# Optimization experiments

Hardware: AMD Instinct MI355X
Metric: run time of the kernel (lower is better)

The kernel has to match this reference:

```python
import jax, jax.numpy as jnp
import numpy as np

B, I, J, P, D = 64, 512, 512, 32, 8
EPS = 1e-5


def _std(t):
    # standardize over last two dims; torch.std uses ddof=1 (unbiased)
    m = t.mean(axis=(-1, -2), keepdims=True)
    s = t.std(axis=(-1, -2), keepdims=True, ddof=1)
    return (t - m) / (s + EPS)


def _flat_softmax(t):
    # softmax over the flattened trailing two dims (torch: flatten(1).softmax(1))
    sh = t.shape
    return jax.nn.softmax(t.reshape(sh[0], sh[1], -1), axis=-1).reshape(sh)


def setup_inputs() -> dict:
    key = jax.random.key(0)
    ks = jax.random.split(key, 10)

    def xav(k, shape):
        # xavier_uniform with relu gain, fan over last two dims
        fan_in, fan_out = shape[-2], shape[-1]
        lim = float(np.sqrt(2.0) * np.sqrt(6.0 / (fan_in + fan_out)))
        return jax.random.uniform(k, shape, jnp.float32, -lim, lim)

    return {
        "x": jax.random.normal(ks[0], (B, I, J), jnp.float32),
        "o_xj": xav(ks[1], (D, J, P)),
        "o_xi": xav(ks[2], (D, I, P)),
        "p_xj": xav(ks[3], (D, I, P)),
        "p_xi": xav(ks[4], (D, J, P)),
        "rel_o_xj": xav(ks[5], (D, J, P)),
        "rel_o_xi": xav(ks[6], (D, I, P)),
        "rel_p_xj": xav(ks[7], (D, P, P)),
        "rel_p_xi": xav(ks[8], (D, P, P)),
        "gamma": jnp.ones((D, 1), jnp.float32),
        "beta": jnp.zeros((D, 1), jnp.float32),
    }


def reference(x, o_xj, o_xi, p_xj, p_xi, rel_o_xj, rel_o_xi, rel_p_xj, rel_p_xi, gamma, beta):
    # Eval-mode reference: dropout is identity. Depth loop vectorized via a leading d axis.
    scale = (I / P) * (J / P)
    x_mean = x.mean(axis=(-1, -2), keepdims=True)[:, None] * scale  # [B,1,1,1]
    x_std = x.std(axis=(-1, -2), keepdims=True, ddof=1)[:, None] * scale

    # relative-mass terms on the original input
    o_rel_xj_sum = _flat_softmax(jnp.einsum('bij,djp->bdip', x, rel_o_xj)).sum(-2)  # [B,D,P]
    o_rel_xi_sum = _flat_softmax(jnp.einsum('bij,dip->bdjp', x, rel_o_xi)).sum(-2)  # [B,D,P]

    # original transforms
    o_t_xj = _std(jnp.tanh(jnp.einsum('bij,djp->bdip', x, o_xj)))   # [B,D,I,P]
    o_t_xi = _std(jnp.tanh(jnp.einsum('bij,dip->bdjp', x, o_xi)))   # [B,D,J,P]

    # permuted transforms -> [B,D,P,P]
    p_t_xj = _std(jnp.tanh(jnp.einsum('bdip,diq->bdpq', o_t_xj, p_xj)))
    p_t_xi = _std(jnp.tanh(jnp.einsum('bdjp,djq->bdqp', o_t_xi, p_xi)))

    # relative-mass terms on the projected tensors
    p_rel_xj_sum = _flat_softmax(jnp.einsum('bdpq,dqr->bdpr', p_t_xj, rel_p_xj)).sum(-2)
    p_rel_xi_sum = _flat_softmax(jnp.einsum('bdpq,dqr->bdpr', p_t_xi, rel_p_xi)).sum(-2)

    fj = jnp.sqrt(o_rel_xj_sum / p_rel_xj_sum)[..., None]  # [B,D,P,1]
    fi = jnp.sqrt(o_rel_xi_sum / p_rel_xi_sum)[..., None]

    xb = jnp.tanh((p_t_xj * fj) * jnp.swapaxes(p_t_xi * fi, -1, -2))
    xb = _std(xb) * x_std + x_mean
    xb = xb * gamma[None, :, :, None] + beta[None, :, :, None]
    return xb.sum(axis=1) / D  # [B,P,P]
```

## Files before the change

kernel.cpp:

```cpp
#include <hip/hip_runtime.h>
#include <math.h>

static constexpr float EPSF = 1e-5f;

typedef short bf16x8 __attribute__((ext_vector_type(8)));
typedef float f32x4 __attribute__((ext_vector_type(4)));
typedef ushort u16x8 __attribute__((ext_vector_type(8)));

__device__ inline ushort bf16rn(float f) {
  unsigned u = __float_as_uint(f);
  unsigned r = (u + 0x7FFFu + ((u >> 16) & 1u)) >> 16;
  return (ushort)r;
}
__device__ inline float bf2f(ushort u) { return __uint_as_float(((unsigned)u) << 16); }
__device__ inline void split2(float f, ushort& hi, ushort& lo) {
  ushort h = bf16rn(f);
  float hf = bf2f(h);
  hi = h;
  lo = bf16rn(f - hf);
}
__device__ inline float fast_tanh(float x) {
  float e = __expf(2.f * x);
  return 1.f - 2.f * __builtin_amdgcn_rcpf(e + 1.f);
}

__device__ inline void gload16(const ushort* g, ushort* l) {
  __builtin_amdgcn_global_load_lds((const __attribute__((address_space(1))) void*)g,
                                   (__attribute__((address_space(3))) void*)l, 16, 0, 0);
}

__device__ inline size_t tiled_addr(int row, int k) {
  return (size_t)(row >> 7) * 65536 + (size_t)(k >> 5) * 4096 +
         (size_t)((k >> 3) & 3) * 1024 + (size_t)(row & 127) * 8 + (k & 7);
}

__global__ __launch_bounds__(256) void conv_pack(
    const float* __restrict__ x,
    const float* __restrict__ o_xj, const float* __restrict__ o_xi,
    const float* __restrict__ rel_o_xj, const float* __restrict__ rel_o_xi,
    const float* __restrict__ p_xj, const float* __restrict__ p_xi,
    ushort* __restrict__ xhi, ushort* __restrict__ xthi,
    ushort* __restrict__ wjhi, ushort* __restrict__ wjlo,
    ushort* __restrict__ wihi, ushort* __restrict__ wilo,
    ushort* __restrict__ Wthi, ushort* __restrict__ Wtlo,
    float* __restrict__ colWs,
    float* __restrict__ bpart) {
  const int bx = blockIdx.x;
  const int tid = threadIdx.x;
  if (bx >= 4352) {
    const int pd = bx - 4352;
    const int path = pd >> 3, d = pd & 7;
    const float* src = (path ? p_xi : p_xj) + (size_t)d * 16384;
    ushort* whi = Wthi + (size_t)pd * 16384;
    ushort* wlo = Wtlo + (size_t)pd * 16384;
    __shared__ float buf[64][33];
    float cw = 0.f;
    const int q = tid >> 3, je8 = (tid & 7) * 8;
    for (int j0 = 0; j0 < 512; j0 += 64) {
      for (int l = tid; l < 2048; l += 256) buf[l >> 5][l & 31] = src[(size_t)j0 * 32 + l];
      __syncthreads();
      u16x8 h8, l8;
      #pragma unroll
      for (int e = 0; e < 8; ++e) {
        float fv = buf[je8 + e][q];
        cw += fv;
        ushort h, l; split2(fv, h, l);
        h8[e] = h; l8[e] = l;
      }
      *reinterpret_cast<u16x8*>(&whi[(size_t)q * 512 + j0 + je8]) = h8;
      *reinterpret_cast<u16x8*>(&wlo[(size_t)q * 512 + j0 + je8]) = l8;
      __syncthreads();
    }
    cw += __shfl_xor(cw, 1); cw += __shfl_xor(cw, 2); cw += __shfl_xor(cw, 4);
    if ((tid & 7) == 0) colWs[(size_t)pd * 32 + q] = cw;
    return;
  }
  if (bx >= 4096) {
    int u = (bx - 4096) * 256 + tid;
    int path = u >> 15;
    int v = u & 32767;
    int c = v >> 6;
    int k0 = (v & 63) * 8;
    int d = c >> 6, s = (c >> 5) & 1, p = c & 31;
    const float* src = path ? (s ? rel_o_xi : o_xi) : (s ? rel_o_xj : o_xj);
    u16x8 h8, l8;
    #pragma unroll
    for (int e = 0; e < 8; ++e) {
      ushort h, l;
      split2(src[((size_t)d * 512 + k0 + e) * 32 + p], h, l);
      h8[e] = h; l8[e] = l;
    }
    size_t a = tiled_addr(c, k0);
    ushort* whi = path ? wihi : wjhi;
    ushort* wlo = path ? wilo : wjlo;
    *reinterpret_cast<u16x8*>(&whi[a]) = h8;
    *reinterpret_cast<u16x8*>(&wlo[a]) = l8;
    return;
  }
  __shared__ float tile[64][65];
  __shared__ float rs[256], rs2[256];
  const int ti = bx & 7, tj = (bx >> 3) & 7, b = bx >> 6;
  const int i0 = ti * 64, j0 = tj * 64;
  const float* xb = x + (size_t)b * 262144;
  const size_t obase = (size_t)b * 262144;
  const int tr = tid >> 4;
  const int tc = (tid & 15) * 4;
  float s = 0.f, s2 = 0.f;
  #pragma unroll
  for (int r = 0; r < 4; ++r) {
    const int row = r * 16 + tr;
    float4 v = *reinterpret_cast<const float4*>(&xb[(size_t)(i0 + row) * 512 + j0 + tc]);
    tile[row][tc + 0] = v.x; tile[row][tc + 1] = v.y;
    tile[row][tc + 2] = v.z; tile[row][tc + 3] = v.w;
    s += v.x + v.y + v.z + v.w;
    s2 += v.x * v.x + v.y * v.y + v.z * v.z + v.w * v.w;
  }
  __syncthreads();
  const int kg = tid >> 5;
  const int rp = tid & 31;
  #pragma unroll
  for (int rr = 0; rr < 2; ++rr) {
    const int li = rp + rr * 32;
    u16x8 h8;
    #pragma unroll
    for (int e = 0; e < 8; ++e) h8[e] = bf16rn(tile[li][kg * 8 + e]);
    *reinterpret_cast<u16x8*>(&xhi[obase + tiled_addr(i0 + li, j0 + kg * 8)]) = h8;
  }
  #pragma unroll
  for (int rr = 0; rr < 2; ++rr) {
    const int lj = rp + rr * 32;
    u16x8 h8;
    #pragma unroll
    for (int e = 0; e < 8; ++e) h8[e] = bf16rn(tile[kg * 8 + e][lj]);
    *reinterpret_cast<u16x8*>(&xthi[obase + tiled_addr(j0 + lj, i0 + kg * 8)]) = h8;
  }
  rs[tid] = s; rs2[tid] = s2;
  __syncthreads();
  for (int off = 128; off > 0; off >>= 1) {
    if (tid < off) { rs[tid] += rs[tid + off]; rs2[tid] += rs2[tid + off]; }
    __syncthreads();
  }
  if (tid == 0) {
    float* pb = bpart + ((size_t)b * 64 + tj * 8 + ti) * 2;
    pb[0] = rs[0]; pb[1] = rs2[0];
  }
}

__global__ __launch_bounds__(256) void mfma_gemm(
    const ushort* __restrict__ xhi, const ushort* __restrict__ xthi,
    const ushort* __restrict__ wjhi, const ushort* __restrict__ wjlo,
    const ushort* __restrict__ wihi, const ushort* __restrict__ wilo,
    ushort* __restrict__ Ttj, ushort* __restrict__ Tti,
    float* __restrict__ pJ, float* __restrict__ pI) {
  const int id = blockIdx.x;
  const int wid = (id & 7) * 256 + (id >> 3);
  const int ct = wid & 3, tm = (wid >> 2) & 3, bz = wid >> 4;
  const int b = bz >> 1, path = bz & 1;
  const ushort* Ahi = (path ? xthi : xhi) + (size_t)b * 262144 + (size_t)tm * 65536;
  const ushort* Bhi = (path ? wihi : wjhi) + (size_t)ct * 65536;
  const ushort* Blo = (path ? wilo : wjlo) + (size_t)ct * 65536;
  ushort* Tb = (path ? Tti : Ttj) + (size_t)b * 131072;
  float* partial = path ? pI : pJ;

  __shared__ alignas(16) ushort As_hi[4096], Bs_hi[4096], Bs_lo[4096];
  __shared__ float rsum[4], rsq[4], rcol[4][32];

  const int tid = threadIdx.x;
  const int lane = tid & 63, w = tid >> 6;
  const int wr = w >> 1, wc = w & 1;
  const int m0 = tm * 128;

  const int L8 = (w * 64 + lane) * 8;
  const int ldsb0 = (w * 64) * 8;
  const int ldsb1 = 2048 + (w * 64) * 8;

  f32x4 acc[4][4] = {};
  const int fr = lane & 15;
  const int kc = lane >> 4;

  for (int ks = 0; ks < 16; ++ks) {
    const ushort* Ah = Ahi + ks * 4096;
    const ushort* Bh = Bhi + ks * 4096;
    const ushort* Bl = Blo + ks * 4096;
    gload16(Ah + L8,        &As_hi[ldsb0]);
    gload16(Ah + 2048 + L8, &As_hi[ldsb1]);
    gload16(Bh + L8,        &Bs_hi[ldsb0]);
    gload16(Bh + 2048 + L8, &Bs_hi[ldsb1]);
    gload16(Bl + L8,        &Bs_lo[ldsb0]);
    gload16(Bl + 2048 + L8, &Bs_lo[ldsb1]);
    __syncthreads();
    bf16x8 ah[4], bh[4], bl2[2];
    #pragma unroll
    for (int mi = 0; mi < 4; ++mi) {
      const int ra = (kc * 128 + wr * 64 + mi * 16 + fr) * 8;
      ah[mi] = *reinterpret_cast<const bf16x8*>(&As_hi[ra]);
    }
    #pragma unroll
    for (int ni = 0; ni < 4; ++ni) {
      const int rb = (kc * 128 + wc * 64 + ni * 16 + fr) * 8;
      bh[ni] = *reinterpret_cast<const bf16x8*>(&Bs_hi[rb]);
      if (ni < 2) bl2[ni] = *reinterpret_cast<const bf16x8*>(&Bs_lo[rb]);
    }
    #pragma unroll
    for (int mi = 0; mi < 4; ++mi) {
      #pragma unroll
      for (int ni = 0; ni < 4; ++ni)
        acc[mi][ni] = __builtin_amdgcn_mfma_f32_16x16x32_bf16(ah[mi], bh[ni], acc[mi][ni], 0, 0, 0);
      #pragma unroll
      for (int ni = 0; ni < 2; ++ni)
        acc[mi][ni] = __builtin_amdgcn_mfma_f32_16x16x32_bf16(ah[mi], bl2[ni], acc[mi][ni], 0, 0, 0);
    }
    __syncthreads();
  }

  float lsum = 0.f, lsq = 0.f, cs0 = 0.f, cs1 = 0.f;
  const int d = ct * 2 + wc;
  #pragma unroll
  for (int mi = 0; mi < 4; ++mi) {
    const int rbase = m0 + wr * 64 + mi * 16 + ((lane >> 4) << 2);
    #pragma unroll
    for (int ni = 0; ni < 4; ++ni) {
      if (ni < 2) {
        const int p = ni * 16 + fr;
        float t0 = fast_tanh(acc[mi][ni][0]);
        float t1 = fast_tanh(acc[mi][ni][1]);
        float t2 = fast_tanh(acc[mi][ni][2]);
        float t3 = fast_tanh(acc[mi][ni][3]);
        lsum += t0 + t1 + t2 + t3;
        lsq += t0 * t0 + t1 * t1 + t2 * t2 + t3 * t3;
        ushort4 pk;
        pk.x = bf16rn(t0); pk.y = bf16rn(t1); pk.z = bf16rn(t2); pk.w = bf16rn(t3);
        *reinterpret_cast<ushort4*>(&Tb[((size_t)d * 32 + p) * 512 + rbase]) = pk;
      } else {
        #pragma unroll
        for (int r = 0; r < 4; ++r) {
          float e = __expf(acc[mi][ni][r]);
          if (ni == 2) cs0 += e; else cs1 += e;
        }
      }
    }
  }
  #pragma unroll
  for (int m = 1; m < 64; m <<= 1) { lsum += __shfl_xor(lsum, m); lsq += __shfl_xor(lsq, m); }
  cs0 += __shfl_xor(cs0, 16); cs0 += __shfl_xor(cs0, 32);
  cs1 += __shfl_xor(cs1, 16); cs1 += __shfl_xor(cs1, 32);
  if (lane == 0) { rsum[w] = lsum; rsq[w] = lsq; }
  if (lane < 16) { rcol[w][lane] = cs0; rcol[w][16 + lane] = cs1; }
  __syncthreads();
  if (tid < 64) {
    const int wc2 = tid >> 5, p = tid & 31;
    float* pb = partial + (((size_t)b * 4 + tm) * 8 + ct * 2 + wc2) * 34;
    pb[2 + p] = rcol[wc2][p] + rcol[wc2 + 2][p];
    if (p == 0) {
      pb[0] = rsum[wc2] + rsum[wc2 + 2];
      pb[1] = rsq[wc2] + rsq[wc2 + 2];
    }
  }
}

__global__ void reduce_stats_kernel(const float* __restrict__ pJ, const float* __restrict__ pI,
                                    float* __restrict__ stats) {
  const int bd = blockIdx.x;
  const int b = bd >> 3, d = bd & 7;
  const int t = threadIdx.x;
  __shared__ float tmp[2][34];
  if (t < 34) {
    float v = 0.f;
    for (int tm = 0; tm < 4; ++tm) v += pJ[(((size_t)b * 4 + tm) * 8 + d) * 34 + t];
    tmp[0][t] = v;
  } else if (t >= 64 && t < 98) {
    const int u = t - 64;
    float v = 0.f;
    for (int tm = 0; tm < 4; ++tm) v += pI[(((size_t)b * 4 + tm) * 8 + d) * 34 + u];
    tmp[1][u] = v;
  }
  __syncthreads();
  if (t < 2) {
    const float* tp = tmp[t];
    float* st = stats + (size_t)bd * 68;
    const float N = 16384.f;
    float mean = tp[0] / N;
    float var = (tp[1] - tp[0] * tp[0] / N) / (N - 1.f);
    float rstd = 1.f / (sqrtf(fmaxf(var, 0.f)) + EPSF);
    st[t * 2 + 0] = mean;
    st[t * 2 + 1] = rstd;
    float tot = 0.f;
    for (int k = 0; k < 32; ++k) tot += tp[2 + k];
    float inv = 1.f / tot;
    for (int k = 0; k < 32; ++k) st[4 + t * 32 + k] = tp[2 + k] * inv;
  }
}

__global__ __launch_bounds__(256) void stage3_fused(
    const ushort* __restrict__ Ttj, const ushort* __restrict__ Tti,
    const ushort* __restrict__ Wthi, const ushort* __restrict__ Wtlo,
    const float* __restrict__ colWs,
    const float* __restrict__ rel_pj, const float* __restrict__ rel_pi,
    const float* __restrict__ stats, const float* __restrict__ bpart,
    const float* __restrict__ gamma_p, const float* __restrict__ beta_p,
    float* __restrict__ xball) {
  const int bd = blockIdx.x;
  const int b = bd >> 3, d = bd & 7;
  const int tid = threadIdx.x;
  const int lane = tid & 63, w = tid >> 6;
  const int path = w >> 1, mt = w & 1;
  const int fr = lane & 15, kg = lane >> 4;

  __shared__ float Vl[2][32][33];
  __shared__ float Rl[2][32][32];
  __shared__ float cred[2][32][33];
  __shared__ float colw_s[64];
  __shared__ float pred[4][2];
  __shared__ float csum[2][32];
  __shared__ float stot[2];
  __shared__ float fsc[2][32];
  __shared__ float red[256], red2[256];
  __shared__ float sred[2], sbst[2];

  for (int l = tid; l < 2048; l += 256) {
    const int pp = l >> 10, idx = l & 1023;
    const float* Rsrc = pp ? rel_pi : rel_pj;
    Rl[pp][idx >> 5][idx & 31] = Rsrc[(size_t)d * 1024 + idx];
  }
  if (tid < 64) colw_s[tid] = colWs[(((size_t)(tid >> 5) * 8 + d)) * 32 + (tid & 31)];
  if (tid >= 128 && tid < 192) {
    const int t = tid - 128;
    float s = bpart[(size_t)b * 128 + t * 2];
    float s2 = bpart[(size_t)b * 128 + t * 2 + 1];
    #pragma unroll
    for (int m = 1; m < 64; m <<= 1) { s += __shfl_xor(s, m); s2 += __shfl_xor(s2, m); }
    if (t == 0) {
      const float N = 262144.f;
      float mean = s / N;
      float var = (s2 - s * s / N) / (N - 1.f);
      sbst[0] = mean * 256.f;
      sbst[1] = sqrtf(fmaxf(var, 0.f)) * 256.f;
    }
  }
  __syncthreads();

  f32x4 acc0 = {}, acc1 = {};
  const ushort* Whi_p = Wthi + ((size_t)path * 8 + d) * 16384;
  const ushort* Wlo_p = Wtlo + ((size_t)path * 8 + d) * 16384;
  const ushort* Tp = (path ? Tti : Ttj) + ((size_t)b * 8 + d) * 16384;

  if (path == 0) {
    const ushort* Arow = Tp + (size_t)(mt * 16 + fr) * 512;
    const ushort* B0h = Whi_p + (size_t)fr * 512;
    const ushort* B0l = Wlo_p + (size_t)fr * 512;
    const ushort* B1h = Whi_p + (size_t)(16 + fr) * 512;
    const ushort* B1l = Wlo_p + (size_t)(16 + fr) * 512;
    for (int k0 = 0; k0 < 512; k0 += 32) {
      const int ko = k0 + kg * 8;
      bf16x8 a   = *reinterpret_cast<const bf16x8*>(Arow + ko);
      bf16x8 b0h = *reinterpret_cast<const bf16x8*>(B0h + ko);
      bf16x8 b0l = *reinterpret_cast<const bf16x8*>(B0l + ko);
      bf16x8 b1h = *reinterpret_cast<const bf16x8*>(B1h + ko);
      bf16x8 b1l = *reinterpret_cast<const bf16x8*>(B1l + ko);
      acc0 = __builtin_amdgcn_mfma_f32_16x16x32_bf16(a, b0h, acc0, 0, 0, 0);
      acc0 = __builtin_amdgcn_mfma_f32_16x16x32_bf16(a, b0l, acc0, 0, 0, 0);
      acc1 = __builtin_amdgcn_mfma_f32_16x16x32_bf16(a, b1h, acc1, 0, 0, 0);
      acc1 = __builtin_amdgcn_mfma_f32_16x16x32_bf16(a, b1l, acc1, 0, 0, 0);
    }
  } else {
    const ushort* Ahr = Whi_p + (size_t)(mt * 16 + fr) * 512;
    const ushort* Alr = Wlo_p + (size_t)(mt * 16 + fr) * 512;
    const ushort* B0 = Tp + (size_t)fr * 512;
    const ushort* B1 = Tp + (size_t)(16 + fr) * 512;
    for (int k0 = 0; k0 < 512; k0 += 32) {
      const int ko = k0 + kg * 8;
      bf16x8 ah = *reinterpret_cast<const bf16x8*>(Ahr + ko);
      bf16x8 al = *reinterpret_cast<const bf16x8*>(Alr + ko);
      bf16x8 b0 = *reinterpret_cast<const bf16x8*>(B0 + ko);
      bf16x8 b1 = *reinterpret_cast<const bf16x8*>(B1 + ko);
      acc0 = __builtin_amdgcn_mfma_f32_16x16x32_bf16(ah, b0, acc0, 0, 0, 0);
      acc0 = __builtin_amdgcn_mfma_f32_16x16x32_bf16(al, b0, acc0, 0, 0, 0);
      acc1 = __builtin_amdgcn_mfma_f32_16x16x32_bf16(ah, b1, acc1, 0, 0, 0);
      acc1 = __builtin_amdgcn_mfma_f32_16x16x32_bf16(al, b1, acc1, 0, 0, 0);
    }
  }

  const float* st = stats + (size_t)bd * 68;
  const float mean = st[path * 2], rstd = st[path * 2 + 1];
  float tv0[4], tv1[4];
  float ls = 0.f, lq = 0.f;
  #pragma unroll
  for (int r = 0; r < 4; ++r) {
    const int rowm = mt * 16 + kg * 4 + r;
    {
      const int col = fr;
      const float cw = (path == 0) ? colw_s[col] : colw_s[32 + rowm];
      float t = fast_tanh((acc0[r] - mean * cw) * rstd);
      tv0[r] = t; ls += t; lq += t * t;
    }
    {
      const int col = 16 + fr;
      const float cw = (path == 0) ? colw_s[col] : colw_s[32 + rowm];
      float t = fast_tanh((acc1[r] - mean * cw) * rstd);
      tv1[r] = t; ls += t; lq += t * t;
    }
  }
  #pragma unroll
  for (int m = 1; m < 64; m <<= 1) { ls += __shfl_xor(ls, m); lq += __shfl_xor(lq, m); }
  if (lane == 0) { pred[w][0] = ls; pred[w][1] = lq; }
  __syncthreads();
  {
    const float S = pred[path * 2][0] + pred[path * 2 + 1][0];
    const float SS = pred[path * 2][1] + pred[path * 2 + 1][1];
    const float m2 = S / 1024.f;
    const float var = (SS - S * S / 1024.f) / 1023.f;
    const float r2 = 1.f / (sqrtf(fmaxf(var, 0.f)) + EPSF);
    #pragma unroll
    for (int r = 0; r < 4; ++r) {
      const int rowm = mt * 16 + kg * 4 + r;
      Vl[path][rowm][fr] = (tv0[r] - m2) * r2;
      Vl[path][rowm][16 + fr] = (tv1[r] - m2) * r2;
    }
  }
  __syncthreads();

  {
    const int t2 = tid & 127;
    const int prow = t2 >> 2, c8 = (t2 & 3) * 8;
    float racc[8] = {};
    #pragma unroll
    for (int c = 0; c < 32; ++c) {
      const float v = Vl[path][prow][c];
      #pragma unroll
      for (int e = 0; e < 8; ++e) racc[e] = fmaf(v, Rl[path][c][c8 + e], racc[e]);
    }
    #pragma unroll
    for (int e = 0; e < 8; ++e) cred[path][prow][c8 + e] = __expf(racc[e]);
  }
  __syncthreads();
  if (tid < 64) {
    const int pp = tid >> 5, q = tid & 31;
    float s = 0.f;
    #pragma unroll 8
    for (int p = 0; p < 32; ++p) s += cred[pp][p][q];
    csum[pp][q] = s;
  }
  __syncthreads();
  if (tid < 2) {
    float tot = 0.f;
    for (int k = 0; k < 32; ++k) tot += csum[tid][k];
    stot[tid] = tot;
  }
  __syncthreads();
  if (tid < 64) {
    const int pp = tid >> 5, q = tid & 31;
    fsc[pp][q] = sqrtf(st[4 + pp * 32 + q] * stot[pp] / csum[pp][q]);
  }
  __syncthreads();

  const int row = tid >> 3, c4 = (tid & 7) * 4;
  float xv[4]; float ls2 = 0.f, lq2 = 0.f;
  #pragma unroll
  for (int e = 0; e < 4; ++e) {
    const int q = c4 + e;
    float v = fast_tanh(Vl[0][row][q] * fsc[0][row] * Vl[1][q][row] * fsc[1][q]);
    xv[e] = v; ls2 += v; lq2 += v * v;
  }
  red[tid] = ls2; red2[tid] = lq2;
  __syncthreads();
  for (int off = 128; off > 0; off >>= 1) {
    if (tid < off) { red[tid] += red[tid + off]; red2[tid] += red2[tid + off]; }
    __syncthreads();
  }
  if (tid == 0) {
    float s = red[0], ss = red2[0];
    float m = s / 1024.f;
    float var = (ss - s * s / 1024.f) / 1023.f;
    sred[0] = m; sred[1] = 1.f / (sqrtf(fmaxf(var, 0.f)) + EPSF);
  }
  __syncthreads();
  const float m3 = sred[0], r3 = sred[1];
  const float xm = sbst[0], xs = sbst[1];
  const float g = gamma_p[d], be = beta_p[d];
  #pragma unroll
  for (int e = 0; e < 4; ++e) {
    float v = (xv[e] - m3) * r3 * xs + xm;
    xball[(size_t)bd * 1024 + row * 32 + c4 + e] = v * g + be;
  }
}

__global__ void final_kernel(const float* __restrict__ xball, float* __restrict__ out) {
  const int b = blockIdx.x;
  for (int e = threadIdx.x; e < 1024; e += 256) {
    float s = 0.f;
    #pragma unroll
    for (int d = 0; d < 8; ++d) s += xball[((size_t)(b * 8 + d)) * 1024 + e];
    out[(size_t)b * 1024 + e] = s * 0.125f;
  }
}

extern "C" void kernel_launch(void* const* d_in, const int* in_sizes, int n_in,
                              void* d_out, int out_size, void* d_ws, size_t ws_size,
                              hipStream_t stream) {
  const float* x        = (const float*)d_in[0];
  const float* o_xj     = (const float*)d_in[1];
  const float* o_xi     = (const float*)d_in[2];
  const float* p_xj     = (const float*)d_in[3];
  const float* p_xi     = (const float*)d_in[4];
  const float* rel_o_xj = (const float*)d_in[5];
  const float* rel_o_xi = (const float*)d_in[6];
  const float* rel_p_xj = (const float*)d_in[7];
  const float* rel_p_xi = (const float*)d_in[8];
  const float* gamma_p  = (const float*)d_in[9];
  const float* beta_p   = (const float*)d_in[10];
  float* out = (float*)d_out;

  char* base = (char*)d_ws;
  ushort* xhi  = (ushort*)base; base += (size_t)33554432;
  ushort* xthi = (ushort*)base; base += (size_t)33554432;
  ushort* wjhi = (ushort*)base; base += 524288;
  ushort* wjlo = (ushort*)base; base += 524288;
  ushort* wihi = (ushort*)base; base += 524288;
  ushort* wilo = (ushort*)base; base += 524288;
  ushort* Ttj  = (ushort*)base; base += (size_t)16777216;
  ushort* Tti  = (ushort*)base; base += (size_t)16777216;
  ushort* Wthi = (ushort*)base; base += 524288;
  ushort* Wtlo = (ushort*)base; base += 524288;
  float* colWs = (float*)base;  base += 2048;
  float* pJ    = (float*)base;  base += 278528;
  float* pI    = (float*)base;  base += 278528;
  float* bpart = (float*)base;  base += 32768;
  float* stats = (float*)base;  base += 139264;
  float* xball = (float*)base;  base += 2097152;

  hipLaunchKernelGGL(conv_pack, dim3(4368), dim3(256), 0, stream,
                     x, o_xj, o_xi, rel_o_xj, rel_o_xi, p_xj, p_xi,
                     xhi, xthi, wjhi, wjlo, wihi, wilo, Wthi, Wtlo, colWs, bpart);
  hipLaunchKernelGGL(mfma_gemm, dim3(2048), dim3(256), 0, stream,
                     xhi, xthi, wjhi, wjlo, wihi, wilo, Ttj, Tti, pJ, pI);
  hipLaunchKernelGGL(reduce_stats_kernel, dim3(512), dim3(128), 0, stream, pJ, pI, stats);
  hipLaunchKernelGGL(stage3_fused, dim3(512), dim3(256), 0, stream,
                     Ttj, Tti, Wthi, Wtlo, colWs, rel_p_xj, rel_p_xi, stats, bpart,
                     gamma_p, beta_p, xball);
  hipLaunchKernelGGL(final_kernel, dim3(64), dim3(256), 0, stream, xball, out);
}
```

Before: 124.4 us.

## Drop bf16 low-part weight correction in first GEMM and fuse stats reduction into stage3

Removes the split hi/lo bf16 representation of the first-stage weights, so the GEMM loads only the high part and issues 16 MFMAs per k-step instead of 24. This cuts LDS traffic, global loads and matrix work in the dominant GEMM. It also deletes the separate reduce_stats kernel and folds the partial-sum reduction and mean/std/softmax normalisation into stage3_fused, saving one launch. The cost is lower weight precision (single bf16 rounding), which may hurt accuracy against the reference.

```diff
diff --git a/kernel.cpp b/kernel.cpp
--- a/kernel.cpp
+++ b/kernel.cpp
@@ -40,8 +40,7 @@
     const float* __restrict__ rel_o_xj, const float* __restrict__ rel_o_xi,
     const float* __restrict__ p_xj, const float* __restrict__ p_xi,
     ushort* __restrict__ xhi, ushort* __restrict__ xthi,
-    ushort* __restrict__ wjhi, ushort* __restrict__ wjlo,
-    ushort* __restrict__ wihi, ushort* __restrict__ wilo,
+    ushort* __restrict__ wjhi, ushort* __restrict__ wihi,
     ushort* __restrict__ Wthi, ushort* __restrict__ Wtlo,
     float* __restrict__ colWs,
     float* __restrict__ bpart) {
@@ -83,18 +82,12 @@
     int k0 = (v & 63) * 8;
     int d = c >> 6, s = (c >> 5) & 1, p = c & 31;
     const float* src = path ? (s ? rel_o_xi : o_xi) : (s ? rel_o_xj : o_xj);
-    u16x8 h8, l8;
-    #pragma unroll
-    for (int e = 0; e < 8; ++e) {
-      ushort h, l;
-      split2(src[((size_t)d * 512 + k0 + e) * 32 + p], h, l);
-      h8[e] = h; l8[e] = l;
-    }
+    u16x8 h8;
+    #pragma unroll
+    for (int e = 0; e < 8; ++e) h8[e] = bf16rn(src[((size_t)d * 512 + k0 + e) * 32 + p]);
     size_t a = tiled_addr(c, k0);
     ushort* whi = path ? wihi : wjhi;
-    ushort* wlo = path ? wilo : wjlo;
     *reinterpret_cast<u16x8*>(&whi[a]) = h8;
-    *reinterpret_cast<u16x8*>(&wlo[a]) = l8;
     return;
   }
   __shared__ float tile[64][65];
@@ -148,8 +141,7 @@
 
 __global__ __launch_bounds__(256) void mfma_gemm(
     const ushort* __restrict__ xhi, const ushort* __restrict__ xthi,
-    const ushort* __restrict__ wjhi, const ushort* __restrict__ wjlo,
-    const ushort* __restrict__ wihi, const ushort* __restrict__ wilo,
+    const ushort* __restrict__ wjhi, const ushort* __restrict__ wihi,
     ushort* __restrict__ Ttj, ushort* __restrict__ Tti,
     float* __restrict__ pJ, float* __restrict__ pI) {
   const int id = blockIdx.x;
@@ -158,11 +150,10 @@
   const int b = bz >> 1, path = bz & 1;
   const ushort* Ahi = (path ? xthi : xhi) + (size_t)b * 262144 + (size_t)tm * 65536;
   const ushort* Bhi = (path ? wihi : wjhi) + (size_t)ct * 65536;
-  const ushort* Blo = (path ? wilo : wjlo) + (size_t)ct * 65536;
   ushort* Tb = (path ? Tti : Ttj) + (size_t)b * 131072;
   float* partial = path ? pI : pJ;
 
-  __shared__ alignas(16) ushort As_hi[4096], Bs_hi[4096], Bs_lo[4096];
+  __shared__ alignas(16) ushort As_hi[4096], Bs_hi[4096];
   __shared__ float rsum[4], rsq[4], rcol[4][32];
 
   const int tid = threadIdx.x;
@@ -181,15 +172,12 @@
   for (int ks = 0; ks < 16; ++ks) {
     const ushort* Ah = Ahi + ks * 4096;
     const ushort* Bh = Bhi + ks * 4096;
-    const ushort* Bl = Blo + ks * 4096;
     gload16(Ah + L8,        &As_hi[ldsb0]);
     gload16(Ah + 2048 + L8, &As_hi[ldsb1]);
     gload16(Bh + L8,        &Bs_hi[ldsb0]);
     gload16(Bh + 2048 + L8, &Bs_hi[ldsb1]);
-    gload16(Bl + L8,        &Bs_lo[ldsb0]);
-    gload16(Bl + 2048 + L8, &Bs_lo[ldsb1]);
     __syncthreads();
-    bf16x8 ah[4], bh[4], bl2[2];
+    bf16x8 ah[4], bh[4];
     #pragma unroll
     for (int mi = 0; mi < 4; ++mi) {
       const int ra = (kc * 128 + wr * 64 + mi * 16 + fr) * 8;
@@ -199,17 +187,12 @@
     for (int ni = 0; ni < 4; ++ni) {
       const int rb = (kc * 128 + wc * 64 + ni * 16 + fr) * 8;
       bh[ni] = *reinterpret_cast<const bf16x8*>(&Bs_hi[rb]);
-      if (ni < 2) bl2[ni] = *reinterpret_cast<const bf16x8*>(&Bs_lo[rb]);
-    }
-    #pragma unroll
-    for (int mi = 0; mi < 4; ++mi) {
+    }
+    #pragma unroll
+    for (int mi = 0; mi < 4; ++mi)
       #pragma unroll
       for (int ni = 0; ni < 4; ++ni)
         acc[mi][ni] = __builtin_amdgcn_mfma_f32_16x16x32_bf16(ah[mi], bh[ni], acc[mi][ni], 0, 0, 0);
-      #pragma unroll
-      for (int ni = 0; ni < 2; ++ni)
-        acc[mi][ni] = __builtin_amdgcn_mfma_f32_16x16x32_bf16(ah[mi], bl2[ni], acc[mi][ni], 0, 0, 0);
-    }
     __syncthreads();
   }
 
@@ -258,45 +241,13 @@
   }
 }
 
-__global__ void reduce_stats_kernel(const float* __restrict__ pJ, const float* __restrict__ pI,
-                                    float* __restrict__ stats) {
-  const int bd = blockIdx.x;
-  const int b = bd >> 3, d = bd & 7;
-  const int t = threadIdx.x;
-  __shared__ float tmp[2][34];
-  if (t < 34) {
-    float v = 0.f;
-    for (int tm = 0; tm < 4; ++tm) v += pJ[(((size_t)b * 4 + tm) * 8 + d) * 34 + t];
-    tmp[0][t] = v;
-  } else if (t >= 64 && t < 98) {
-    const int u = t - 64;
-    float v = 0.f;
-    for (int tm = 0; tm < 4; ++tm) v += pI[(((size_t)b * 4 + tm) * 8 + d) * 34 + u];
-    tmp[1][u] = v;
-  }
-  __syncthreads();
-  if (t < 2) {
-    const float* tp = tmp[t];
-    float* st = stats + (size_t)bd * 68;
-    const float N = 16384.f;
-    float mean = tp[0] / N;
-    float var = (tp[1] - tp[0] * tp[0] / N) / (N - 1.f);
-    float rstd = 1.f / (sqrtf(fmaxf(var, 0.f)) + EPSF);
-    st[t * 2 + 0] = mean;
-    st[t * 2 + 1] = rstd;
-    float tot = 0.f;
-    for (int k = 0; k < 32; ++k) tot += tp[2 + k];
-    float inv = 1.f / tot;
-    for (int k = 0; k < 32; ++k) st[4 + t * 32 + k] = tp[2 + k] * inv;
-  }
-}
-
 __global__ __launch_bounds__(256) void stage3_fused(
     const ushort* __restrict__ Ttj, const ushort* __restrict__ Tti,
     const ushort* __restrict__ Wthi, const ushort* __restrict__ Wtlo,
     const float* __restrict__ colWs,
     const float* __restrict__ rel_pj, const float* __restrict__ rel_pi,
-    const float* __restrict__ stats, const float* __restrict__ bpart,
+    const float* __restrict__ pJ, const float* __restrict__ pI,
+    const float* __restrict__ bpart,
     const float* __restrict__ gamma_p, const float* __restrict__ beta_p,
     float* __restrict__ xball) {
   const int bd = blockIdx.x;
@@ -310,6 +261,9 @@
   __shared__ float Rl[2][32][32];
   __shared__ float cred[2][32][33];
   __shared__ float colw_s[64];
+  __shared__ float stS[2][34];
+  __shared__ float ms[2][2];
+  __shared__ float orelT[2];
   __shared__ float pred[4][2];
   __shared__ float csum[2][32];
   __shared__ float stot[2];
@@ -323,8 +277,17 @@
     Rl[pp][idx >> 5][idx & 31] = Rsrc[(size_t)d * 1024 + idx];
   }
   if (tid < 64) colw_s[tid] = colWs[(((size_t)(tid >> 5) * 8 + d)) * 32 + (tid & 31)];
-  if (tid >= 128 && tid < 192) {
-    const int t = tid - 128;
+  if (tid >= 64 && tid < 132) {
+    const int u = tid - 64;
+    const int pp = u >= 34, t = pp ? u - 34 : u;
+    const float* P = pp ? pI : pJ;
+    float v = 0.f;
+    #pragma unroll
+    for (int tm2 = 0; tm2 < 4; ++tm2) v += P[(((size_t)b * 4 + tm2) * 8 + d) * 34 + t];
+    stS[pp][t] = v;
+  }
+  if (tid >= 192) {
+    const int t = tid - 192;
     float s = bpart[(size_t)b * 128 + t * 2];
     float s2 = bpart[(size_t)b * 128 + t * 2 + 1];
     #pragma unroll
@@ -338,6 +301,17 @@
     }
   }
   __syncthreads();
+  if (tid < 2) {
+    const float* S = stS[tid];
+    const float N = 16384.f;
+    float mean = S[0] / N;
+    float var = (S[1] - S[0] * S[0] / N) / (N - 1.f);
+    ms[tid][0] = mean;
+    ms[tid][1] = 1.f / (sqrtf(fmaxf(var, 0.f)) + EPSF);
+    float tot = 0.f;
+    for (int k = 0; k < 32; ++k) tot += S[2 + k];
+    orelT[tid] = tot;
+  }
 
   f32x4 acc0 = {}, acc1 = {};
   const ushort* Whi_p = Wthi + ((size_t)path * 8 + d) * 16384;
@@ -379,23 +353,21 @@
       acc1 = __builtin_amdgcn_mfma_f32_16x16x32_bf16(al, b1, acc1, 0, 0, 0);
     }
   }
-
-  const float* st = stats + (size_t)bd * 68;
-  const float mean = st[path * 2], rstd = st[path * 2 + 1];
+  __syncthreads();
+
+  const float mean = ms[path][0], rstd = ms[path][1];
   float tv0[4], tv1[4];
   float ls = 0.f, lq = 0.f;
   #pragma unroll
   for (int r = 0; r < 4; ++r) {
     const int rowm = mt * 16 + kg * 4 + r;
     {
-      const int col = fr;
-      const float cw = (path == 0) ? colw_s[col] : colw_s[32 + rowm];
+      const float cw = (path == 0) ? colw_s[fr] : colw_s[32 + rowm];
       float t = fast_tanh((acc0[r] - mean * cw) * rstd);
       tv0[r] = t; ls += t; lq += t * t;
     }
     {
-      const int col = 16 + fr;
-      const float cw = (path == 0) ? colw_s[col] : colw_s[32 + rowm];
+      const float cw = (path == 0) ? colw_s[16 + fr] : colw_s[32 + rowm];
       float t = fast_tanh((acc1[r] - mean * cw) * rstd);
       tv1[r] = t; ls += t; lq += t * t;
     }
@@ -449,7 +421,7 @@
   __syncthreads();
   if (tid < 64) {
     const int pp = tid >> 5, q = tid & 31;
-    fsc[pp][q] = sqrtf(st[4 + pp * 32 + q] * stot[pp] / csum[pp][q]);
+    fsc[pp][q] = sqrtf((stS[pp][2 + q] / orelT[pp]) * stot[pp] / csum[pp][q]);
   }
   __syncthreads();
 
@@ -514,9 +486,7 @@
   ushort* xhi  = (ushort*)base; base += (size_t)33554432;
   ushort* xthi = (ushort*)base; base += (size_t)33554432;
   ushort* wjhi = (ushort*)base; base += 524288;
-  ushort* wjlo = (ushort*)base; base += 524288;
   ushort* wihi = (ushort*)base; base += 524288;
-  ushort* wilo = (ushort*)base; base += 524288;
   ushort* Ttj  = (ushort*)base; base += (size_t)16777216;
   ushort* Tti  = (ushort*)base; base += (size_t)16777216;
   ushort* Wthi = (ushort*)base; base += 524288;
@@ -525,17 +495,15 @@
   float* pJ    = (float*)base;  base += 278528;
   float* pI    = (float*)base;  base += 278528;
   float* bpart = (float*)base;  base += 32768;
-  float* stats = (float*)base;  base += 139264;
   float* xball = (float*)base;  base += 2097152;
 
   hipLaunchKernelGGL(conv_pack, dim3(4368), dim3(256), 0, stream,
                      x, o_xj, o_xi, rel_o_xj, rel_o_xi, p_xj, p_xi,
-                     xhi, xthi, wjhi, wjlo, wihi, wilo, Wthi, Wtlo, colWs, bpart);
+                     xhi, xthi, wjhi, wihi, Wthi, Wtlo, colWs, bpart);
   hipLaunchKernelGGL(mfma_gemm, dim3(2048), dim3(256), 0, stream,
-                     xhi, xthi, wjhi, wjlo, wihi, wilo, Ttj, Tti, pJ, pI);
-  hipLaunchKernelGGL(reduce_stats_kernel, dim3(512), dim3(128), 0, stream, pJ, pI, stats);
+                     xhi, xthi, wjhi, wihi, Ttj, Tti, pJ, pI);
   hipLaunchKernelGGL(stage3_fused, dim3(512), dim3(256), 0, stream,
-                     Ttj, Tti, Wthi, Wtlo, colWs, rel_p_xj, rel_p_xi, stats, bpart,
+                     Ttj, Tti, Wthi, Wtlo, colWs, rel_p_xj, rel_p_xi, pJ, pI, bpart,
                      gamma_p, beta_p, xball);
   hipLaunchKernelGGL(final_kernel, dim3(64), dim3(256), 0, stream, xball, out);
 }
```

After: 106.0 us. 14.8% less time.
